# Kernel tuning notes

Measured on AMD Instinct MI355X. Metric: run time of the kernel, lower is better.

## Reference

```python
import jax, jax.numpy as jnp
import numpy as np

BS, NUM_RELS, NUM_NODES, EMB = 8, 16, 512, 256


def setup_inputs() -> dict:
    key = jax.random.key(0)
    k1, k2, k3, k4 = jax.random.split(key, 4)
    features = jax.random.normal(k1, (BS, NUM_NODES, EMB), dtype=jnp.float32)
    adjacency = jax.random.uniform(k2, (BS, NUM_RELS, NUM_NODES, NUM_NODES), dtype=jnp.float32)
    # xavier_uniform bounds
    bound = float(np.sqrt(6.0 / (EMB + EMB)))
    W_r = jax.random.uniform(k3, (NUM_RELS, EMB, EMB), minval=-bound, maxval=bound, dtype=jnp.float32)
    W_0 = jax.random.uniform(k4, (EMB, EMB), minval=-bound, maxval=bound, dtype=jnp.float32)
    return {"features": features, "adjacency": adjacency, "W_r": W_r, "W_0": W_0}


def reference(features, adjacency, W_r, W_0):
    # msg[b,r,n,d] = sum_m adjacency[b,r,n,m] * features[b,m,d]
    msg = jnp.einsum('brnm,bmd->brnd', adjacency, features)
    # per-relation projection then sum over relations: [b,n,h]
    features_1 = jnp.einsum('brnd,rdh->bnh', msg, W_r)
    features_2 = jnp.einsum('bnd,dh->bnh', features, W_0)
    return jax.nn.relu(features_1 + features_2)
```

## Files before the change

kernel.cpp:

```cpp
#include <hip/hip_runtime.h>
#include <hip/hip_bf16.h>

#define BS   8
#define NREL 16
#define NN   512
#define EMB  256

typedef float f32x4 __attribute__((ext_vector_type(4)));
typedef short s16x8 __attribute__((ext_vector_type(8)));

__device__ __forceinline__ unsigned short f2bf_bits(float f) {
    union { float f; unsigned u; } v; v.f = f;
    unsigned r = (v.u + 0x7FFFu + ((v.u >> 16) & 1u)) >> 16;
    return (unsigned short)r;
}

__device__ __forceinline__ unsigned short f2bf_hw(float f) {
    union { __hip_bfloat16 h; unsigned short u; } v;
    v.h = __float2bfloat16(f);
    return v.u;
}

__global__ __launch_bounds__(256) void k0_transpose(
        const float* __restrict__ Wr, const float* __restrict__ W0,
        unsigned short* __restrict__ wT) {
    __shared__ float tile[32][33];
    int bid = blockIdx.x;
    int rel = bid / 64;
    int t   = bid % 64;
    int d0  = (t & 7) * 32;
    int h0  = (t >> 3) * 32;
    int tx  = threadIdx.x & 31;
    int ty  = threadIdx.x >> 5;
    const float* src = (rel < NREL) ? (Wr + rel * (EMB * EMB)) : W0;
#pragma unroll
    for (int k = 0; k < 4; ++k) {
        int d = d0 + ty + k * 8;
        tile[ty + k * 8][tx] = src[d * EMB + h0 + tx];
    }
    __syncthreads();
#pragma unroll
    for (int k = 0; k < 4; ++k) {
        int h = h0 + ty + k * 8;
        wT[(rel * EMB + h) * EMB + d0 + tx] = f2bf_bits(tile[tx][ty + k * 8]);
    }
}

__global__ __launch_bounds__(256) void k0b_convF(
        const float* __restrict__ F, unsigned short* __restrict__ Fbf) {
    long i = ((long)blockIdx.x * 256 + threadIdx.x) * 8;
    f32x4 x0 = *(const f32x4*)(F + i);
    f32x4 x1 = *(const f32x4*)(F + i + 4);
    s16x8 v;
    v[0] = (short)f2bf_bits(x0[0]); v[1] = (short)f2bf_bits(x0[1]);
    v[2] = (short)f2bf_bits(x0[2]); v[3] = (short)f2bf_bits(x0[3]);
    v[4] = (short)f2bf_bits(x1[0]); v[5] = (short)f2bf_bits(x1[1]);
    v[6] = (short)f2bf_bits(x1[2]); v[7] = (short)f2bf_bits(x1[3]);
    *(s16x8*)(Fbf + i) = v;
}

__global__ __launch_bounds__(256) void k1_fw(
        const unsigned short* __restrict__ Fbf, const unsigned short* __restrict__ wT,
        unsigned short* __restrict__ FW, float* __restrict__ F2f) {
    int bid = blockIdx.x;
    int b   = bid & 7;
    int q   = bid >> 3;
    int rel = q % 17;
    int mt  = q / 17;
    int tid = threadIdx.x;
    int w   = tid >> 6;
    int l   = tid & 63;
    int lg  = l >> 4;
    int lr  = l & 15;

    int h0 = w * 64;
    int m0 = mt * 64;

    const unsigned short* wt = wT + rel * (EMB * EMB);
    const unsigned short* Fb = Fbf + (long)b * (NN * EMB);

    f32x4 acc[4][4];
#pragma unroll
    for (int i = 0; i < 4; ++i)
#pragma unroll
        for (int j = 0; j < 4; ++j) acc[i][j] = (f32x4){0.f, 0.f, 0.f, 0.f};

#pragma unroll 2
    for (int kk = 0; kk < EMB; kk += 32) {
        s16x8 afrag[4];
#pragma unroll
        for (int hi = 0; hi < 4; ++hi) {
            int row = h0 + hi * 16 + lr;
            afrag[hi] = *(const s16x8*)(wt + row * EMB + kk + lg * 8);
        }
        s16x8 bfrag[4];
#pragma unroll
        for (int bi = 0; bi < 4; ++bi) {
            int m = m0 + bi * 16 + lr;
            bfrag[bi] = *(const s16x8*)(Fb + m * EMB + kk + lg * 8);
        }
#pragma unroll
        for (int hi = 0; hi < 4; ++hi)
#pragma unroll
            for (int bi = 0; bi < 4; ++bi)
                acc[hi][bi] = __builtin_amdgcn_mfma_f32_16x16x32_bf16(
                    afrag[hi], bfrag[bi], acc[hi][bi], 0, 0, 0);
    }

#pragma unroll
    for (int hi = 0; hi < 4; ++hi) {
#pragma unroll
        for (int bi = 0; bi < 4; ++bi) {
            int m  = m0 + bi * 16 + lr;
            int kg = m >> 3, ko = m & 7;
#pragma unroll
            for (int j = 0; j < 4; ++j) {
                int h = h0 + hi * 16 + lg * 4 + j;
                if (rel < NREL)
                    FW[(long)((b * 16 + rel) * 64 + kg) * 2048 + h * 8 + ko] =
                        f2bf_bits(acc[hi][bi][j]);
                else
                    F2f[((long)b * NN + m) * EMB + h] = acc[hi][bi][j];
            }
        }
    }
}

__global__ __launch_bounds__(256, 2) void k2_main(
        const float* __restrict__ adj, const unsigned short* __restrict__ FW,
        float* __restrict__ part) {
    __shared__ unsigned short Blds[2][2][8192];
    int bid = blockIdx.x;
    int b   = bid & 7;
    int t   = bid >> 3;
    int nt  = t & 7;
    int rg  = t >> 3;
    int tid = threadIdx.x;
    int w   = tid >> 6;
    int l   = tid & 63;
    int lg  = l >> 4, lr = l & 15;
    int wr  = w >> 1;
    int wc  = w & 1;

    int nrow = nt * 64 + wr * 32;

    f32x4 acc0[16], acc1[16];
#pragma unroll
    for (int i = 0; i < 16; ++i) {
        acc0[i] = (f32x4){0.f, 0.f, 0.f, 0.f};
        acc1[i] = (f32x4){0.f, 0.f, 0.f, 0.f};
    }

    const float* adjb0 =
        adj + (((long)(b * 16 + rg * 2)) * NN + nrow + lr) * NN + lg * 8;
    const float* adjb1 = adjb0 + 16 * NN;
    const unsigned short* fwb = FW + (long)(b * 16 + rg * 2) * 131072;

    int sp = w & 1;
    int hf = w >> 1;
    const unsigned short* fw_s = fwb + hf * 4096 + l * 8;
    unsigned short* st0 = &Blds[0][sp][hf * 4096 + l * 8];
    unsigned short* st1 = &Blds[1][sp][hf * 4096 + l * 8];

    s16x8 fwr[8];
    f32x4 ax[2][2], ay[2][2];

#define SOFF(sl) ((long)((sl) >> 4) * 131072 + ((sl) & 15) * 8192)

    {
        const unsigned short* s = fw_s + SOFF(sp);
#pragma unroll
        for (int k = 0; k < 8; ++k) fwr[k] = *(const s16x8*)(s + k * 512);
#pragma unroll
        for (int k = 0; k < 8; ++k) *(s16x8*)(st0 + k * 512) = fwr[k];
    }
    {
        const float* p0 = adjb0 + wc * 32;
        const float* p1 = adjb1 + wc * 32;
        ax[0][0] = *(const f32x4*)p0; ay[0][0] = *(const f32x4*)(p0 + 4);
        ax[0][1] = *(const f32x4*)p1; ay[0][1] = *(const f32x4*)(p1 + 4);
    }
    {
        const unsigned short* s = fw_s + SOFF(2 + sp);
#pragma unroll
        for (int k = 0; k < 8; ++k) fwr[k] = *(const s16x8*)(s + k * 512);
    }
    asm volatile("s_waitcnt lgkmcnt(0)" ::: "memory");
    __builtin_amdgcn_sched_barrier(0);
    __builtin_amdgcn_s_barrier();
    asm volatile("" ::: "memory");

#pragma unroll
    for (int i = 0; i < 16; ++i) {
        if (i + 1 < 16) {
            int sl = 2 * (i + 1) + wc;
            long ao = (long)(sl >> 4) * (NN * NN) + (sl & 15) * 32;
            const float* p0 = adjb0 + ao;
            const float* p1 = adjb1 + ao;
            if (((i + 1) & 1) == 0) {
                ax[0][0] = *(const f32x4*)p0; ay[0][0] = *(const f32x4*)(p0 + 4);
                ax[0][1] = *(const f32x4*)p1; ay[0][1] = *(const f32x4*)(p1 + 4);
            } else {
                ax[1][0] = *(const f32x4*)p0; ay[1][0] = *(const f32x4*)(p0 + 4);
                ax[1][1] = *(const f32x4*)p1; ay[1][1] = *(const f32x4*)(p1 + 4);
            }
        }

        f32x4 x00 = ax[i & 1][0], x01 = ay[i & 1][0];
        f32x4 x10 = ax[i & 1][1], x11 = ay[i & 1][1];
        s16x8 a0, a1;
        a0[0] = (short)f2bf_hw(x00[0]); a0[1] = (short)f2bf_hw(x00[1]);
        a0[2] = (short)f2bf_hw(x00[2]); a0[3] = (short)f2bf_hw(x00[3]);
        a0[4] = (short)f2bf_hw(x01[0]); a0[5] = (short)f2bf_hw(x01[1]);
        a0[6] = (short)f2bf_hw(x01[2]); a0[7] = (short)f2bf_hw(x01[3]);
        a1[0] = (short)f2bf_hw(x10[0]); a1[1] = (short)f2bf_hw(x10[1]);
        a1[2] = (short)f2bf_hw(x10[2]); a1[3] = (short)f2bf_hw(x10[3]);
        a1[4] = (short)f2bf_hw(x11[0]); a1[5] = (short)f2bf_hw(x11[1]);
        a1[6] = (short)f2bf_hw(x11[2]); a1[7] = (short)f2bf_hw(x11[3]);

        const unsigned short* bl = &Blds[i & 1][wc][lg * 2048];
#pragma unroll
        for (int f = 0; f < 16; ++f) {
            s16x8 bf = *(const s16x8*)(bl + (f * 16 + lr) * 8);
            acc0[f] = __builtin_amdgcn_mfma_f32_16x16x32_bf16(a0, bf, acc0[f], 0, 0, 0);
            acc1[f] = __builtin_amdgcn_mfma_f32_16x16x32_bf16(a1, bf, acc1[f], 0, 0, 0);
        }
        asm volatile("" ::: "memory");

        if (i + 1 < 16) {
            unsigned short* dst = ((i + 1) & 1) ? st1 : st0;
#pragma unroll
            for (int k = 0; k < 8; ++k) *(s16x8*)(dst + k * 512) = fwr[k];
            if (i + 2 < 16) {
                const unsigned short* s = fw_s + SOFF(2 * (i + 2) + sp);
#pragma unroll
                for (int k = 0; k < 8; ++k) fwr[k] = *(const s16x8*)(s + k * 512);
            }
            asm volatile("s_waitcnt lgkmcnt(0)" ::: "memory");
            __builtin_amdgcn_sched_barrier(0);
            __builtin_amdgcn_s_barrier();
            asm volatile("" ::: "memory");
        }
    }
#undef SOFF

    __syncthreads();
    float* lf = (float*)Blds;
    if (wc == 1) {
#pragma unroll
        for (int g = 0; g < 2; ++g)
#pragma unroll
            for (int f = 0; f < 16; ++f)
#pragma unroll
                for (int j = 0; j < 4; ++j)
                    lf[wr * 8192 + ((g * 16 + f) * 4 + j) * 64 + l] =
                        g ? acc1[f][j] : acc0[f][j];
    }
    __syncthreads();
    if (wc == 0) {
        float* pp = part + ((long)rg * BS + b) * (NN * EMB);
#pragma unroll
        for (int g = 0; g < 2; ++g)
#pragma unroll
            for (int f = 0; f < 16; ++f) {
                int h = f * 16 + lr;
#pragma unroll
                for (int j = 0; j < 4; ++j) {
                    int n = nrow + g * 16 + lg * 4 + j;
                    float v = (g ? acc1[f][j] : acc0[f][j]) +
                              lf[wr * 8192 + ((g * 16 + f) * 4 + j) * 64 + l];
                    pp[(long)n * EMB + h] = v;
                }
            }
    }
}

__global__ __launch_bounds__(256) void k3_reduce(
        const float* __restrict__ part, const float* __restrict__ F2f,
        float* __restrict__ out) {
    const long PS = (long)BS * NN * EMB;
    long i = ((long)blockIdx.x * 256 + threadIdx.x) * 4;
    f32x4 s = *(const f32x4*)(part + i);
#pragma unroll
    for (int rg = 1; rg < 8; ++rg)
        s += *(const f32x4*)(part + i + (long)rg * PS);
    s += *(const f32x4*)(F2f + i);
    f32x4 r;
#pragma unroll
    for (int j = 0; j < 4; ++j) r[j] = s[j] > 0.f ? s[j] : 0.f;
    *(f32x4*)(out + i) = r;
}

extern "C" void kernel_launch(void* const* d_in, const int* in_sizes, int n_in,
                              void* d_out, int out_size, void* d_ws, size_t ws_size,
                              hipStream_t stream) {
    const float* F   = (const float*)d_in[0];
    const float* adj = (const float*)d_in[1];
    const float* Wr  = (const float*)d_in[2];
    const float* W0  = (const float*)d_in[3];
    float* out = (float*)d_out;

    unsigned short* wT  = (unsigned short*)d_ws;
    unsigned short* Fbf = wT + 17 * 256 * 256;
    unsigned short* FW  = Fbf + (long)8 * 512 * 256;
    float* F2f  = (float*)(FW + (long)8 * 16 * 64 * 2048);
    float* part = F2f + (long)8 * 512 * 256;

    k0_transpose<<<17 * 64, 256, 0, stream>>>(Wr, W0, wT);
    k0b_convF<<<512, 256, 0, stream>>>(F, Fbf);
    k1_fw<<<1088, 256, 0, stream>>>(Fbf, wT, FW, F2f);
    k2_main<<<512, 256, 0, stream>>>(adj, FW, part);
    k3_reduce<<<1024, 256, 0, stream>>>(part, F2f, out);
}
```

Measured before the change: 105.7 us.

## Load B fragments directly from global memory instead of LDS double buffering

The main kernel no longer stages the pre-packed bf16 FW operand through a double-buffered LDS ring with per-iteration barriers. Each wave now reads its 16 B fragments straight from global memory (relying on L2 caching across the waves that share them) at the start of each k-step. This removes the LDS stores, the LDS reads and the block-wide barrier on every step. In exchange it adds global-memory traffic and latency: the loads are not prefetched ahead of the MFMAs and 16 extra vector registers are live, which may expose memory latency.

```diff
diff --git a/kernel.cpp b/kernel.cpp
--- a/kernel.cpp
+++ b/kernel.cpp
@@ -129,7 +129,7 @@
 __global__ __launch_bounds__(256, 2) void k2_main(
         const float* __restrict__ adj, const unsigned short* __restrict__ FW,
         float* __restrict__ part) {
-    __shared__ unsigned short Blds[2][2][8192];
+    __shared__ float lf[16384];
     int bid = blockIdx.x;
     int b   = bid & 7;
     int t   = bid >> 3;
@@ -154,47 +154,31 @@
     const float* adjb0 =
         adj + (((long)(b * 16 + rg * 2)) * NN + nrow + lr) * NN + lg * 8;
     const float* adjb1 = adjb0 + 16 * NN;
-    const unsigned short* fwb = FW + (long)(b * 16 + rg * 2) * 131072;
-
-    int sp = w & 1;
-    int hf = w >> 1;
-    const unsigned short* fw_s = fwb + hf * 4096 + l * 8;
-    unsigned short* st0 = &Blds[0][sp][hf * 4096 + l * 8];
-    unsigned short* st1 = &Blds[1][sp][hf * 4096 + l * 8];
-
-    s16x8 fwr[8];
+    const unsigned short* fwb =
+        FW + (long)(b * 16 + rg * 2) * 131072 + lg * 2048 + lr * 8;
+
     f32x4 ax[2][2], ay[2][2];
 
-#define SOFF(sl) ((long)((sl) >> 4) * 131072 + ((sl) & 15) * 8192)
-
-    {
-        const unsigned short* s = fw_s + SOFF(sp);
-#pragma unroll
-        for (int k = 0; k < 8; ++k) fwr[k] = *(const s16x8*)(s + k * 512);
-#pragma unroll
-        for (int k = 0; k < 8; ++k) *(s16x8*)(st0 + k * 512) = fwr[k];
-    }
     {
         const float* p0 = adjb0 + wc * 32;
         const float* p1 = adjb1 + wc * 32;
         ax[0][0] = *(const f32x4*)p0; ay[0][0] = *(const f32x4*)(p0 + 4);
         ax[0][1] = *(const f32x4*)p1; ay[0][1] = *(const f32x4*)(p1 + 4);
     }
-    {
-        const unsigned short* s = fw_s + SOFF(2 + sp);
-#pragma unroll
-        for (int k = 0; k < 8; ++k) fwr[k] = *(const s16x8*)(s + k * 512);
-    }
-    asm volatile("s_waitcnt lgkmcnt(0)" ::: "memory");
-    __builtin_amdgcn_sched_barrier(0);
-    __builtin_amdgcn_s_barrier();
-    asm volatile("" ::: "memory");
 
 #pragma unroll
     for (int i = 0; i < 16; ++i) {
+        int sl = 2 * i + wc;
+        const unsigned short* pk =
+            fwb + (long)(sl >> 4) * 131072 + ((sl & 15) * 4) * 2048;
+        s16x8 bfr[16];
+#pragma unroll
+        for (int f = 0; f < 16; ++f)
+            bfr[f] = *(const s16x8*)(pk + f * 128);
+
         if (i + 1 < 16) {
-            int sl = 2 * (i + 1) + wc;
-            long ao = (long)(sl >> 4) * (NN * NN) + (sl & 15) * 32;
+            int sn = 2 * (i + 1) + wc;
+            long ao = (long)(sn >> 4) * (NN * NN) + (sn & 15) * 32;
             const float* p0 = adjb0 + ao;
             const float* p1 = adjb1 + ao;
             if (((i + 1) & 1) == 0) {
@@ -218,34 +202,14 @@
         a1[4] = (short)f2bf_hw(x11[0]); a1[5] = (short)f2bf_hw(x11[1]);
         a1[6] = (short)f2bf_hw(x11[2]); a1[7] = (short)f2bf_hw(x11[3]);
 
-        const unsigned short* bl = &Blds[i & 1][wc][lg * 2048];
 #pragma unroll
         for (int f = 0; f < 16; ++f) {
-            s16x8 bf = *(const s16x8*)(bl + (f * 16 + lr) * 8);
-            acc0[f] = __builtin_amdgcn_mfma_f32_16x16x32_bf16(a0, bf, acc0[f], 0, 0, 0);
-            acc1[f] = __builtin_amdgcn_mfma_f32_16x16x32_bf16(a1, bf, acc1[f], 0, 0, 0);
-        }
-        asm volatile("" ::: "memory");
-
-        if (i + 1 < 16) {
-            unsigned short* dst = ((i + 1) & 1) ? st1 : st0;
-#pragma unroll
-            for (int k = 0; k < 8; ++k) *(s16x8*)(dst + k * 512) = fwr[k];
-            if (i + 2 < 16) {
-                const unsigned short* s = fw_s + SOFF(2 * (i + 2) + sp);
-#pragma unroll
-                for (int k = 0; k < 8; ++k) fwr[k] = *(const s16x8*)(s + k * 512);
-            }
-            asm volatile("s_waitcnt lgkmcnt(0)" ::: "memory");
-            __builtin_amdgcn_sched_barrier(0);
-            __builtin_amdgcn_s_barrier();
-            asm volatile("" ::: "memory");
-        }
-    }
-#undef SOFF
+            acc0[f] = __builtin_amdgcn_mfma_f32_16x16x32_bf16(a0, bfr[f], acc0[f], 0, 0, 0);
+            acc1[f] = __builtin_amdgcn_mfma_f32_16x16x32_bf16(a1, bfr[f], acc1[f], 0, 0, 0);
+        }
+    }
 
     __syncthreads();
-    float* lf = (float*)Blds;
     if (wc == 1) {
 #pragma unroll
         for (int g = 0; g < 2; ++g)
```

Measured after the change: 126.8 us. +20.0%, slower.

## Widen main GEMM blocks to 512 threads sharing FW tiles, fuse prep kernels

Applied to the files above, without the earlier changes.

The main adjacency-times-FW kernel now runs 256 blocks of 512 threads, each covering 128 node rows instead of 64. All eight waves share the same FW slab staged in LDS, which halves the global FW traffic per output row, and the epilogue reduction is split into two passes to fit the smaller LDS buffer. The two prep kernels (weight transpose and feature bf16 conversion) are merged into one launch, and the k1 K-loop is rewritten with explicit double-buffered register fragments. The risks are fewer blocks for the CUs to spread across, higher register pressure with 512 threads and launch bounds of 2, and an extra barrier in the epilogue.

```diff
diff --git a/kernel.cpp b/kernel.cpp
--- a/kernel.cpp
+++ b/kernel.cpp
@@ -21,42 +21,42 @@
     return v.u;
 }
 
-__global__ __launch_bounds__(256) void k0_transpose(
+__global__ __launch_bounds__(256) void k0_prep(
         const float* __restrict__ Wr, const float* __restrict__ W0,
-        unsigned short* __restrict__ wT) {
-    __shared__ float tile[32][33];
+        const float* __restrict__ F,
+        unsigned short* __restrict__ wT, unsigned short* __restrict__ Fbf) {
     int bid = blockIdx.x;
-    int rel = bid / 64;
-    int t   = bid % 64;
-    int d0  = (t & 7) * 32;
-    int h0  = (t >> 3) * 32;
-    int tx  = threadIdx.x & 31;
-    int ty  = threadIdx.x >> 5;
-    const float* src = (rel < NREL) ? (Wr + rel * (EMB * EMB)) : W0;
-#pragma unroll
-    for (int k = 0; k < 4; ++k) {
-        int d = d0 + ty + k * 8;
-        tile[ty + k * 8][tx] = src[d * EMB + h0 + tx];
-    }
-    __syncthreads();
-#pragma unroll
-    for (int k = 0; k < 4; ++k) {
-        int h = h0 + ty + k * 8;
-        wT[(rel * EMB + h) * EMB + d0 + tx] = f2bf_bits(tile[tx][ty + k * 8]);
-    }
-}
-
-__global__ __launch_bounds__(256) void k0b_convF(
-        const float* __restrict__ F, unsigned short* __restrict__ Fbf) {
-    long i = ((long)blockIdx.x * 256 + threadIdx.x) * 8;
-    f32x4 x0 = *(const f32x4*)(F + i);
-    f32x4 x1 = *(const f32x4*)(F + i + 4);
-    s16x8 v;
-    v[0] = (short)f2bf_bits(x0[0]); v[1] = (short)f2bf_bits(x0[1]);
-    v[2] = (short)f2bf_bits(x0[2]); v[3] = (short)f2bf_bits(x0[3]);
-    v[4] = (short)f2bf_bits(x1[0]); v[5] = (short)f2bf_bits(x1[1]);
-    v[6] = (short)f2bf_bits(x1[2]); v[7] = (short)f2bf_bits(x1[3]);
-    *(s16x8*)(Fbf + i) = v;
+    if (bid < 1088) {
+        __shared__ float tile[32][33];
+        int rel = bid / 64;
+        int t   = bid % 64;
+        int d0  = (t & 7) * 32;
+        int h0  = (t >> 3) * 32;
+        int tx  = threadIdx.x & 31;
+        int ty  = threadIdx.x >> 5;
+        const float* src = (rel < NREL) ? (Wr + rel * (EMB * EMB)) : W0;
+#pragma unroll
+        for (int k = 0; k < 4; ++k) {
+            int d = d0 + ty + k * 8;
+            tile[ty + k * 8][tx] = src[d * EMB + h0 + tx];
+        }
+        __syncthreads();
+#pragma unroll
+        for (int k = 0; k < 4; ++k) {
+            int h = h0 + ty + k * 8;
+            wT[(rel * EMB + h) * EMB + d0 + tx] = f2bf_bits(tile[tx][ty + k * 8]);
+        }
+    } else {
+        long i = ((long)(bid - 1088) * 256 + threadIdx.x) * 8;
+        f32x4 x0 = *(const f32x4*)(F + i);
+        f32x4 x1 = *(const f32x4*)(F + i + 4);
+        s16x8 v;
+        v[0] = (short)f2bf_bits(x0[0]); v[1] = (short)f2bf_bits(x0[1]);
+        v[2] = (short)f2bf_bits(x0[2]); v[3] = (short)f2bf_bits(x0[3]);
+        v[4] = (short)f2bf_bits(x1[0]); v[5] = (short)f2bf_bits(x1[1]);
+        v[6] = (short)f2bf_bits(x1[2]); v[7] = (short)f2bf_bits(x1[3]);
+        *(s16x8*)(Fbf + i) = v;
+    }
 }
 
 __global__ __launch_bounds__(256) void k1_fw(
@@ -76,8 +76,8 @@
     int h0 = w * 64;
     int m0 = mt * 64;
 
-    const unsigned short* wt = wT + rel * (EMB * EMB);
-    const unsigned short* Fb = Fbf + (long)b * (NN * EMB);
+    const unsigned short* wt = wT + rel * (EMB * EMB) + lg * 8;
+    const unsigned short* Fb = Fbf + (long)b * (NN * EMB) + lg * 8;
 
     f32x4 acc[4][4];
 #pragma unroll
@@ -85,26 +85,32 @@
 #pragma unroll
         for (int j = 0; j < 4; ++j) acc[i][j] = (f32x4){0.f, 0.f, 0.f, 0.f};
 
-#pragma unroll 2
-    for (int kk = 0; kk < EMB; kk += 32) {
-        s16x8 afrag[4];
-#pragma unroll
-        for (int hi = 0; hi < 4; ++hi) {
-            int row = h0 + hi * 16 + lr;
-            afrag[hi] = *(const s16x8*)(wt + row * EMB + kk + lg * 8);
-        }
-        s16x8 bfrag[4];
-#pragma unroll
-        for (int bi = 0; bi < 4; ++bi) {
-            int m = m0 + bi * 16 + lr;
-            bfrag[bi] = *(const s16x8*)(Fb + m * EMB + kk + lg * 8);
+    s16x8 afr[2][4], bfr[2][4];
+#pragma unroll
+    for (int hi = 0; hi < 4; ++hi)
+        afr[0][hi] = *(const s16x8*)(wt + (h0 + hi * 16 + lr) * EMB);
+#pragma unroll
+    for (int bi = 0; bi < 4; ++bi)
+        bfr[0][bi] = *(const s16x8*)(Fb + (m0 + bi * 16 + lr) * EMB);
+
+#pragma unroll
+    for (int kk = 0; kk < 8; ++kk) {
+        int cur = kk & 1, nxt = cur ^ 1;
+        if (kk < 7) {
+            int ko = (kk + 1) * 32;
+#pragma unroll
+            for (int hi = 0; hi < 4; ++hi)
+                afr[nxt][hi] = *(const s16x8*)(wt + (h0 + hi * 16 + lr) * EMB + ko);
+#pragma unroll
+            for (int bi = 0; bi < 4; ++bi)
+                bfr[nxt][bi] = *(const s16x8*)(Fb + (m0 + bi * 16 + lr) * EMB + ko);
         }
 #pragma unroll
         for (int hi = 0; hi < 4; ++hi)
 #pragma unroll
             for (int bi = 0; bi < 4; ++bi)
                 acc[hi][bi] = __builtin_amdgcn_mfma_f32_16x16x32_bf16(
-                    afrag[hi], bfrag[bi], acc[hi][bi], 0, 0, 0);
+                    afr[cur][hi], bfr[cur][bi], acc[hi][bi], 0, 0, 0);
     }
 
 #pragma unroll
@@ -126,15 +132,15 @@
     }
 }
 
-__global__ __launch_bounds__(256, 2) void k2_main(
+__global__ __launch_bounds__(512, 2) void k2_main(
         const float* __restrict__ adj, const unsigned short* __restrict__ FW,
         float* __restrict__ part) {
-    __shared__ unsigned short Blds[2][2][8192];
+    __shared__ unsigned short Blds[2][16384];
     int bid = blockIdx.x;
     int b   = bid & 7;
     int t   = bid >> 3;
-    int nt  = t & 7;
-    int rg  = t >> 3;
+    int nt  = t & 3;
+    int rg  = t >> 2;
     int tid = threadIdx.x;
     int w   = tid >> 6;
     int l   = tid & 63;
@@ -142,7 +148,7 @@
     int wr  = w >> 1;
     int wc  = w & 1;
 
-    int nrow = nt * 64 + wr * 32;
+    int nrow = nt * 128 + wr * 32;
 
     f32x4 acc0[16], acc1[16];
 #pragma unroll
@@ -156,23 +162,18 @@
     const float* adjb1 = adjb0 + 16 * NN;
     const unsigned short* fwb = FW + (long)(b * 16 + rg * 2) * 131072;
 
-    int sp = w & 1;
-    int hf = w >> 1;
-    const unsigned short* fw_s = fwb + hf * 4096 + l * 8;
-    unsigned short* st0 = &Blds[0][sp][hf * 4096 + l * 8];
-    unsigned short* st1 = &Blds[1][sp][hf * 4096 + l * 8];
-
-    s16x8 fwr[8];
+    s16x8 fwr[4];
     f32x4 ax[2][2], ay[2][2];
 
-#define SOFF(sl) ((long)((sl) >> 4) * 131072 + ((sl) & 15) * 8192)
+#define POFF(p) ((long)((p) >> 3) * 131072 + ((p) & 7) * 16384)
 
     {
-        const unsigned short* s = fw_s + SOFF(sp);
-#pragma unroll
-        for (int k = 0; k < 8; ++k) fwr[k] = *(const s16x8*)(s + k * 512);
-#pragma unroll
-        for (int k = 0; k < 8; ++k) *(s16x8*)(st0 + k * 512) = fwr[k];
+        const unsigned short* s = fwb + POFF(0) + tid * 8;
+#pragma unroll
+        for (int c = 0; c < 4; ++c) fwr[c] = *(const s16x8*)(s + c * 4096);
+#pragma unroll
+        for (int c = 0; c < 4; ++c)
+            *(s16x8*)(&Blds[0][c * 4096 + tid * 8]) = fwr[c];
     }
     {
         const float* p0 = adjb0 + wc * 32;
@@ -181,9 +182,9 @@
         ax[0][1] = *(const f32x4*)p1; ay[0][1] = *(const f32x4*)(p1 + 4);
     }
     {
-        const unsigned short* s = fw_s + SOFF(2 + sp);
-#pragma unroll
-        for (int k = 0; k < 8; ++k) fwr[k] = *(const s16x8*)(s + k * 512);
+        const unsigned short* s = fwb + POFF(1) + tid * 8;
+#pragma unroll
+        for (int c = 0; c < 4; ++c) fwr[c] = *(const s16x8*)(s + c * 4096);
     }
     asm volatile("s_waitcnt lgkmcnt(0)" ::: "memory");
     __builtin_amdgcn_sched_barrier(0);
@@ -218,7 +219,7 @@
         a1[4] = (short)f2bf_hw(x11[0]); a1[5] = (short)f2bf_hw(x11[1]);
         a1[6] = (short)f2bf_hw(x11[2]); a1[7] = (short)f2bf_hw(x11[3]);
 
-        const unsigned short* bl = &Blds[i & 1][wc][lg * 2048];
+        const unsigned short* bl = &Blds[i & 1][wc * 8192 + lg * 2048];
 #pragma unroll
         for (int f = 0; f < 16; ++f) {
             s16x8 bf = *(const s16x8*)(bl + (f * 16 + lr) * 8);
@@ -228,13 +229,13 @@
         asm volatile("" ::: "memory");
 
         if (i + 1 < 16) {
-            unsigned short* dst = ((i + 1) & 1) ? st1 : st0;
-#pragma unroll
-            for (int k = 0; k < 8; ++k) *(s16x8*)(dst + k * 512) = fwr[k];
+            unsigned short* dst = &Blds[(i + 1) & 1][tid * 8];
+#pragma unroll
+            for (int c = 0; c < 4; ++c) *(s16x8*)(dst + c * 4096) = fwr[c];
             if (i + 2 < 16) {
-                const unsigned short* s = fw_s + SOFF(2 * (i + 2) + sp);
-#pragma unroll
-                for (int k = 0; k < 8; ++k) fwr[k] = *(const s16x8*)(s + k * 512);
+                const unsigned short* s = fwb + POFF(i + 2) + tid * 8;
+#pragma unroll
+                for (int c = 0; c < 4; ++c) fwr[c] = *(const s16x8*)(s + c * 4096);
             }
             asm volatile("s_waitcnt lgkmcnt(0)" ::: "memory");
             __builtin_amdgcn_sched_barrier(0);
@@ -242,25 +243,23 @@
             asm volatile("" ::: "memory");
         }
     }
-#undef SOFF
-
-    __syncthreads();
+#undef POFF
+
     float* lf = (float*)Blds;
-    if (wc == 1) {
-#pragma unroll
-        for (int g = 0; g < 2; ++g)
+    float* pp = part + ((long)rg * BS + b) * (NN * EMB);
+#pragma unroll
+    for (int g = 0; g < 2; ++g) {
+        __syncthreads();
+        if (wc == 1) {
 #pragma unroll
             for (int f = 0; f < 16; ++f)
 #pragma unroll
                 for (int j = 0; j < 4; ++j)
-                    lf[wr * 8192 + ((g * 16 + f) * 4 + j) * 64 + l] =
+                    lf[wr * 4096 + (f * 4 + j) * 64 + l] =
                         g ? acc1[f][j] : acc0[f][j];
-    }
-    __syncthreads();
-    if (wc == 0) {
-        float* pp = part + ((long)rg * BS + b) * (NN * EMB);
-#pragma unroll
-        for (int g = 0; g < 2; ++g)
+        }
+        __syncthreads();
+        if (wc == 0) {
 #pragma unroll
             for (int f = 0; f < 16; ++f) {
                 int h = f * 16 + lr;
@@ -268,10 +267,11 @@
                 for (int j = 0; j < 4; ++j) {
                     int n = nrow + g * 16 + lg * 4 + j;
                     float v = (g ? acc1[f][j] : acc0[f][j]) +
-                              lf[wr * 8192 + ((g * 16 + f) * 4 + j) * 64 + l];
+                              lf[wr * 4096 + (f * 4 + j) * 64 + l];
                     pp[(long)n * EMB + h] = v;
                 }
             }
+        }
     }
 }
 
@@ -306,9 +306,8 @@
     float* F2f  = (float*)(FW + (long)8 * 16 * 64 * 2048);
     float* part = F2f + (long)8 * 512 * 256;
 
-    k0_transpose<<<17 * 64, 256, 0, stream>>>(Wr, W0, wT);
-    k0b_convF<<<512, 256, 0, stream>>>(F, Fbf);
+    k0_prep<<<1600, 256, 0, stream>>>(Wr, W0, F, wT, Fbf);
     k1_fw<<<1088, 256, 0, stream>>>(Fbf, wT, FW, F2f);
-    k2_main<<<512, 256, 0, stream>>>(adj, FW, part);
+    k2_main<<<256, 512, 0, stream>>>(adj, FW, part);
     k3_reduce<<<1024, 256, 0, stream>>>(part, F2f, out);
 }
```

After: 99.09 us. -6.2%, faster.
